# Performance work log

Hardware: AMD Instinct MI355X
Metric: run time of the kernel (lower is better)

The kernel has to match this reference:

```python
import jax, jax.numpy as jnp
import numpy as np
import math

D_MODEL = 768
D_STATE = 16
D_CONV = 4
EXPAND = 2
D_INNER = EXPAND * D_MODEL
DT_RANK = math.ceil(D_MODEL / 16)
B_SZ, SEQ = 2, 2048


def setup_inputs() -> dict:
    key = jax.random.key(0)
    ks = jax.random.split(key, 10)
    s = 0.02
    inp = {
        "input_states": jax.random.normal(ks[0], (B_SZ, SEQ, D_MODEL), jnp.float32),
        "in_proj_w": jax.random.normal(ks[1], (2 * D_INNER, D_MODEL), jnp.float32) * s,
        "conv_w": jax.random.normal(ks[2], (D_INNER, 1, D_CONV), jnp.float32) * s,
        "conv_b": jnp.zeros((D_INNER,), jnp.float32),
        "x_proj_w": jax.random.normal(ks[3], (DT_RANK + 2 * D_STATE, D_INNER), jnp.float32) * s,
        "dt_proj_w": jax.random.normal(ks[4], (D_INNER, DT_RANK), jnp.float32) * s,
        "dt_proj_b": jax.random.normal(ks[5], (D_INNER,), jnp.float32) * 0.1,
        # S4D-real style init: A_log = log(1..d_state) per channel
        "A_log": jnp.log(jnp.broadcast_to(jnp.arange(1, D_STATE + 1, dtype=jnp.float32), (D_INNER, D_STATE))),
        "D": jnp.ones((D_INNER,), jnp.float32),
        "out_proj_w": jax.random.normal(ks[6], (D_MODEL, D_INNER), jnp.float32) * s,
        "context_len": 2,
    }
    return inp


def _silu(x):
    return x * jax.nn.sigmoid(x)


def _chain_tree_scan(w, x):
    # first-order linear recurrence h_t = w_t * h_{t-1} + x_t along last axis
    # (w_0 is ignored by construction of the associative combine)
    def comb(l, r):
        al, bl = l
        ar, br = r
        return (ar * al, ar * bl + br)
    _, h = jax.lax.associative_scan(comb, (w, x), axis=-1)
    return h


def reference(input_states, in_proj_w, conv_w, conv_b, x_proj_w,
              dt_proj_w, dt_proj_b, A_log, D, out_proj_w, context_len):
    # context_len == 2 -> chain-tree branch (identity BFS order, parent[i]=i-1)
    b, L, dm = input_states.shape
    di, n = A_log.shape[0], A_log.shape[1]

    proj = jnp.einsum('bld,ed->ble', input_states, in_proj_w)  # [b,l,2*di]
    proj = jnp.transpose(proj, (0, 2, 1))                      # [b,2*di,l]
    hidden, gate = jnp.split(proj, 2, axis=1)                  # each [b,di,l]

    # causal depthwise conv1d (pad left d_conv-1, truncate to seq_len)
    hidden = jax.lax.conv_general_dilated(
        hidden, conv_w, window_strides=(1,), padding=[(D_CONV - 1, 0)],
        dimension_numbers=('NCH', 'OIH', 'NCH'), feature_group_count=di)
    hidden = _silu(hidden + conv_b[None, :, None])             # [b,di,l]

    ssm = jnp.einsum('bdl,ed->ble', hidden, x_proj_w)          # [b,l,dt_rank+2n]
    dt, Bm, Cm = jnp.split(ssm, [DT_RANK, DT_RANK + n], axis=-1)
    dt = jax.nn.softplus(jnp.einsum('blr,dr->bld', dt, dt_proj_w) + dt_proj_b)
    dt = jnp.transpose(dt, (0, 2, 1))                          # [b,di,l]

    A = -jnp.exp(A_log.astype(jnp.float32))                    # [di,n]
    dA = jnp.exp(A[None, :, None, :] * dt[:, :, :, None])      # [b,di,l,n]
    dBu = dt[:, :, :, None] * Bm[:, None, :, :] * hidden[:, :, :, None]  # [b,di,l,n]

    # rearrange 'b d l n -> b (d n) l'
    w = jnp.transpose(dA, (0, 1, 3, 2)).reshape(b, di * n, L)
    fin = jnp.transpose(dBu, (0, 1, 3, 2)).reshape(b, di * n, L)

    fin_f = jnp.flip(fin, axis=-1)
    w_f = jnp.roll(jnp.flip(w, axis=-1), 1, axis=-1)

    h = _chain_tree_scan(w_f, fin_f)
    # feature_out2 (edge_weight == w_f via identity gather) * 0.3 + feature_out1
    fout = 1.3 * h

    fout = jnp.flip(fout, axis=-1)                              # [b,(d n),l]
    fout = fout.reshape(b, di, n, L)
    fout = jnp.transpose(fout, (0, 3, 1, 2))                    # [b,l,d,n]

    scan_out = jnp.einsum('bldn,bln->bld', fout, Cm)            # [b,l,di]
    scan_out = jnp.transpose(scan_out, (0, 2, 1))               # [b,di,l]

    y = scan_out + hidden * D[None, :, None]
    y = y * _silu(gate)
    out = jnp.einsum('bdl,ed->ble', y, out_proj_w)              # [b,l,d_model]
    return out
```

## Files before the change

kernel.cpp:

```cpp
#include <hip/hip_runtime.h>
#include <hip/hip_bf16.h>

#define DI     1536
#define DM     768
#define E2     3072
#define NST    16
#define LSEQ   2048
#define NB     2
#define NLB    4096
#define SSMW   80
#define DTRANK 48
#define NC     32
#define CP     64
#define LOG2E  1.44269504f
#define RLOG2E 0.69314718f

typedef unsigned short u16;
typedef unsigned int   u32;
typedef __attribute__((ext_vector_type(8))) __bf16 bf16x8;
typedef __attribute__((ext_vector_type(4))) float  f32x4;

__device__ __forceinline__ float b2f(u16 u) {
  union { u32 i; float f; } v; v.i = ((u32)u) << 16; return v.f;
}
__device__ __forceinline__ u16 f2b(float f) {
  union { float f; u32 i; } v; v.f = f;
  u32 r = v.i + 0x7FFFu + ((v.i >> 16) & 1u);
  return (u16)(r >> 16);
}
__device__ __forceinline__ void gld16(const u16* g, u16* l) {
  __builtin_amdgcn_global_load_lds(
      (const __attribute__((address_space(1))) void*)g,
      (__attribute__((address_space(3))) void*)l, 16, 0, 0);
}
__device__ __forceinline__ float silu_f(float x) {
  return x / (1.f + __expf(-x));
}
__device__ __forceinline__ float fexp2(float x) { return __builtin_amdgcn_exp2f(x); }
__device__ __forceinline__ float flog2(float x) { return __builtin_amdgcn_logf(x); }
__device__ __forceinline__ float softplus_f(float x) {
  return (x > 20.f) ? x : flog2(1.f + fexp2(x * LOG2E)) * RLOG2E;
}

#define ROWSUM16(p)                                                                \
  asm("v_add_f32 %0, %0, %0 row_ror:8 row_mask:0xf bank_mask:0xf" : "+v"(p));      \
  asm("v_add_f32 %0, %0, %0 row_ror:4 row_mask:0xf bank_mask:0xf" : "+v"(p));      \
  asm("v_add_f32 %0, %0, %0 row_ror:2 row_mask:0xf bank_mask:0xf" : "+v"(p));      \
  asm("v_add_f32 %0, %0, %0 row_ror:1 row_mask:0xf bank_mask:0xf" : "+v"(p));

__global__ __launch_bounds__(256) void castall(const float* __restrict__ x_in,
                                               const float* __restrict__ w_in,
                                               const float* __restrict__ w_out,
                                               const float* __restrict__ w_x,
                                               const float* __restrict__ w_dt,
                                               const float* __restrict__ b_dt,
                                               u16* __restrict__ in_b,
                                               u16* __restrict__ win_b,
                                               u16* __restrict__ wout_b,
                                               u16* __restrict__ wx_b,
                                               u16* __restrict__ wdtp_b) {
  int i = (blockIdx.x * 256 + threadIdx.x) * 4;
  const int n1 = NLB * DM, n2 = n1 + E2 * DM, n3 = n2 + DM * DI, n4 = n3 + SSMW * DI;
  const int n5 = n4 + DI * 64;
  if (i >= n5) return;
  if (i >= n4) {
    int off = i - n4;
    u16 o[4];
#pragma unroll
    for (int j = 0; j < 4; j++) {
      int row = (off + j) >> 6, col = (off + j) & 63;
      float v = (col < 48) ? w_dt[row * 48 + col] : (col == 48 ? b_dt[row] : 0.f);
      o[j] = f2b(v);
    }
    uint2 pk; pk.x = (u32)o[0] | ((u32)o[1] << 16); pk.y = (u32)o[2] | ((u32)o[3] << 16);
    *(uint2*)(wdtp_b + off) = pk;
    return;
  }
  const float* src; u16* dst; int off;
  if (i < n1)      { src = x_in;  dst = in_b;   off = i; }
  else if (i < n2) { src = w_in;  dst = win_b;  off = i - n1; }
  else if (i < n3) { src = w_out; dst = wout_b; off = i - n2; }
  else             { src = w_x;   dst = wx_b;   off = i - n3; }
  float4 v = *(const float4*)(src + off);
  u32 lo = (u32)f2b(v.x) | ((u32)f2b(v.y) << 16);
  u32 hi = (u32)f2b(v.z) | ((u32)f2b(v.w) << 16);
  uint2 pk; pk.x = lo; pk.y = hi;
  *(uint2*)(dst + off) = pk;
}

template<int CMODE>
__global__ __launch_bounds__(256) void gemm_bt(const u16* __restrict__ A,
                                               const u16* __restrict__ B,
                                               void* __restrict__ Cp,
                                               int M, int N, int K) {
  __shared__ __align__(16) u16 a_s[128 * 32];
  __shared__ __align__(16) u16 b_s[128 * 32];
  const int tid = threadIdx.x, lane = tid & 63, w = tid >> 6;
  const int m0 = blockIdx.x * 128, n0 = blockIdx.y * 128;
  const int wm = w >> 1, wn = w & 1;
  f32x4 acc[4][4];
#pragma unroll
  for (int i = 0; i < 4; i++)
#pragma unroll
    for (int j = 0; j < 4; j++) acc[i][j] = (f32x4){0.f, 0.f, 0.f, 0.f};

  const int rA = lane >> 2;
  const int c8 = (lane & 3) * 8;
  const int fr = lane & 15;
  const int fk = (lane >> 4) * 8;

  for (int k0 = 0; k0 < K; k0 += 32) {
#pragma unroll
    for (int j = 0; j < 2; j++) {
      int rr = (w * 2 + j) * 16;
      gld16(A + (size_t)(m0 + rr + rA) * K + k0 + c8, a_s + rr * 32);
      gld16(B + (size_t)(n0 + rr + rA) * K + k0 + c8, b_s + rr * 32);
    }
    __syncthreads();
    bf16x8 af[4], bf[4];
#pragma unroll
    for (int mi = 0; mi < 4; mi++)
      af[mi] = *(const bf16x8*)(a_s + (wm * 64 + mi * 16 + fr) * 32 + fk);
#pragma unroll
    for (int ni = 0; ni < 4; ni++)
      bf[ni] = *(const bf16x8*)(b_s + (wn * 64 + ni * 16 + fr) * 32 + fk);
#pragma unroll
    for (int mi = 0; mi < 4; mi++)
#pragma unroll
      for (int ni = 0; ni < 4; ni++)
        acc[mi][ni] = __builtin_amdgcn_mfma_f32_16x16x32_bf16(
            af[mi], bf[ni], acc[mi][ni], 0, 0, 0);
    __syncthreads();
  }

  const int rbase = (lane >> 4) * 4, cbase = lane & 15;
#pragma unroll
  for (int mi = 0; mi < 4; mi++)
#pragma unroll
    for (int ni = 0; ni < 4; ni++)
#pragma unroll
      for (int j = 0; j < 4; j++) {
        int m = m0 + wm * 64 + mi * 16 + rbase + j;
        int n = n0 + wn * 64 + ni * 16 + cbase;
        float v = acc[mi][ni][j];
        if (CMODE == 0) {
          u16* C = (u16*)Cp;
          C[((size_t)(n >> 11) * E2 + m) * LSEQ + (n & 2047)] = f2b(v);
        } else {
          float* C = (float*)Cp;
          C[(size_t)m * N + n] = v;
        }
      }
}

__global__ __launch_bounds__(256) void gemm_xproj(const u16* __restrict__ A,
                                                  const u16* __restrict__ B,
                                                  float* __restrict__ C,
                                                  u16* __restrict__ dtin) {
  __shared__ __align__(16) u16 a_s[128 * 32];
  __shared__ __align__(16) u16 b_s[128 * 32];
  const int tid = threadIdx.x, lane = tid & 63, w = tid >> 6;
  const int n0 = blockIdx.x * 128;
  const int K = DI;
  f32x4 acc[5][2];
#pragma unroll
  for (int i = 0; i < 5; i++) { acc[i][0] = (f32x4){0,0,0,0}; acc[i][1] = (f32x4){0,0,0,0}; }

  const int rA = lane >> 2;
  const int c8 = (lane & 3) * 8;
  const int fr = lane & 15;
  const int fk = (lane >> 4) * 8;

  for (int k0 = 0; k0 < K; k0 += 32) {
#pragma unroll
    for (int j = 0; j < 2; j++) {
      int rr = (w * 2 + j) * 16;
      gld16(A + (size_t)(rr + rA) * K + k0 + c8, a_s + rr * 32);
      gld16(B + (size_t)(n0 + rr + rA) * K + k0 + c8, b_s + rr * 32);
    }
    __syncthreads();
    bf16x8 af[5], bf[2];
#pragma unroll
    for (int mi = 0; mi < 5; mi++)
      af[mi] = *(const bf16x8*)(a_s + (mi * 16 + fr) * 32 + fk);
#pragma unroll
    for (int ni = 0; ni < 2; ni++)
      bf[ni] = *(const bf16x8*)(b_s + (w * 32 + ni * 16 + fr) * 32 + fk);
#pragma unroll
    for (int mi = 0; mi < 5; mi++)
#pragma unroll
      for (int ni = 0; ni < 2; ni++)
        acc[mi][ni] = __builtin_amdgcn_mfma_f32_16x16x32_bf16(
            af[mi], bf[ni], acc[mi][ni], 0, 0, 0);
    __syncthreads();
  }

  const int rbase = (lane >> 4) * 4, cbase = lane & 15;
#pragma unroll
  for (int mi = 0; mi < 5; mi++)
#pragma unroll
    for (int ni = 0; ni < 2; ni++)
#pragma unroll
      for (int j = 0; j < 4; j++) {
        int m = mi * 16 + rbase + j;
        int n = n0 + w * 32 + ni * 16 + cbase;
        float v = acc[mi][ni][j];
        C[(size_t)n * SSMW + m] = v;
        if (m < 64) {
          u16 dv = (m < 48) ? f2b(v) : (m == 48 ? f2b(1.0f) : (u16)0);
          dtin[(size_t)n * 64 + m] = dv;
        }
      }
}

__global__ __launch_bounds__(256) void conv_silu(const u16* __restrict__ proj,
                                                 const float* __restrict__ cw,
                                                 const float* __restrict__ cb,
                                                 u16* __restrict__ hidden) {
  __shared__ __align__(16) u16 in_s[64][96];
  __shared__ __align__(16) u16 o_s[64][64];
  const int t = threadIdx.x;
  const int d0 = blockIdx.x * 64, l0 = blockIdx.y * 64, bb = blockIdx.z;

  for (int c = t; c < 64 * 12; c += 256) {
    int r = c / 12, q = c % 12;
    int gl = l0 - 32 + q * 8;
    uint4 v;
    if (gl >= 0) v = *(const uint4*)(proj + ((size_t)bb * E2 + d0 + r) * LSEQ + gl);
    else         v = (uint4){0u, 0u, 0u, 0u};
    *(uint4*)(&in_s[r][q * 8]) = v;
  }
  __syncthreads();

  const int dd = t >> 2, ls = t & 3;
  const int d = d0 + dd;
  const float w0 = cw[d * 4 + 0], w1 = cw[d * 4 + 1], w2 = cw[d * 4 + 2], w3 = cw[d * 4 + 3];
  const float bias = cb[d];
#pragma unroll
  for (int i = 0; i < 16; i++) {
    int li = ls * 16 + i;
    int base = 32 + li - 3;
    float h = w0 * b2f(in_s[dd][base + 0]) + w1 * b2f(in_s[dd][base + 1]) +
              w2 * b2f(in_s[dd][base + 2]) + w3 * b2f(in_s[dd][base + 3]) + bias;
    o_s[li][dd] = f2b(silu_f(h));
  }
  __syncthreads();

  for (int c = t; c < 512; c += 256) {
    int r = c >> 3, q = c & 7;
    *(uint4*)(hidden + ((size_t)bb * LSEQ + l0 + r) * DI + d0 + q * 8) =
        *(const uint4*)(&o_s[r][q * 8]);
  }
}


#define DT_TILE_MFMA(dtin, wdtp)                                                          \
  {                                                                                       \
    const u16* ar = dtin + ((size_t)bb * LSEQ + l0) * 64;                                 \
    bf16x8 wb0 = *(const bf16x8*)(wdtp + (size_t)(d0 + fr) * 64 + fk);                    \
    bf16x8 wb1 = *(const bf16x8*)(wdtp + (size_t)(d0 + fr) * 64 + 32 + fk);               \
    for (int mt = wv; mt < 5; mt += 4) {                                                  \
      bf16x8 a0 = *(const bf16x8*)(ar + (size_t)(mt * 16 + fr) * 64 + fk);                \
      bf16x8 a1 = *(const bf16x8*)(ar + (size_t)(mt * 16 + fr) * 64 + 32 + fk);           \
      f32x4 da = (f32x4){0.f, 0.f, 0.f, 0.f};                                             \
      da = __builtin_amdgcn_mfma_f32_16x16x32_bf16(a0, wb0, da, 0, 0, 0);                 \
      da = __builtin_amdgcn_mfma_f32_16x16x32_bf16(a1, wb1, da, 0, 0, 0);                 \
      _Pragma("unroll")                                                                   \
      for (int j = 0; j < 4; j++)                                                         \
        dt_f[cbase][mt * 16 + rbase + j] = softplus_f(da[j]);                             \
    }                                                                                     \
  }

__global__ __launch_bounds__(256) void scan_sum(const u16* __restrict__ dtin,
                                                const u16* __restrict__ wdtp,
                                                const u16* __restrict__ hidden,
                                                const float* __restrict__ ssm,
                                                const float* __restrict__ A_log,
                                                float* __restrict__ gsum,
                                                float* __restrict__ sdt) {
  __shared__ __align__(16) float dt_f[16][84];
  __shared__ __align__(16) float hid_f[16][68];
  __shared__ __align__(16) float B_t[16][68];
  const int t = threadIdx.x;
  const int d0 = blockIdx.x * 16, c = blockIdx.y, bb = blockIdx.z;
  const int dl = t >> 4, n = t & 15;
  const int d = d0 + dl;
  const int l0 = c * CP;
  const int lane = t & 63, wv = t >> 6;
  const int fr = lane & 15, fk = (lane >> 4) * 8;
  const int rbase = (lane >> 4) * 4, cbase = lane & 15;
  {
    int r = t >> 2, q = t & 3;
    size_t lbrow = (size_t)bb * LSEQ + l0 + r;
    uint2 hv = *(const uint2*)(hidden + lbrow * DI + d0 + q * 4);
    float4 bv = *(const float4*)(ssm + lbrow * SSMW + 48 + q * 4);
    hid_f[q * 4 + 0][r] = b2f((u16)hv.x); hid_f[q * 4 + 1][r] = b2f((u16)(hv.x >> 16));
    hid_f[q * 4 + 2][r] = b2f((u16)hv.y); hid_f[q * 4 + 3][r] = b2f((u16)(hv.y >> 16));
    B_t[q * 4 + 0][r] = bv.x; B_t[q * 4 + 1][r] = bv.y;
    B_t[q * 4 + 2][r] = bv.z; B_t[q * 4 + 3][r] = bv.w;
  }
  DT_TILE_MFMA(dtin, wdtp)
  const float An2 = -__expf(A_log[d * 16 + n]) * LOG2E;
  __syncthreads();
  float dt_prev = (c == NC - 1) ? 0.f : dt_f[dl][64];
  float g = 0.f, sumdt = 0.f;
#define STEPS(dtv_, hv_, Bv_) {            \
    float dtv = dtv_;                      \
    float dA = fexp2(An2 * dt_prev);       \
    g = dtv * (Bv_) * (hv_) + dA * g;      \
    sumdt += dt_prev;                      \
    dt_prev = dtv; }
#pragma unroll
  for (int s = 7; s >= 0; --s) {
    f32x4 t0 = *(const f32x4*)(&dt_f[dl][s * 8]);
    f32x4 t1 = *(const f32x4*)(&dt_f[dl][s * 8 + 4]);
    f32x4 h0 = *(const f32x4*)(&hid_f[dl][s * 8]);
    f32x4 h1 = *(const f32x4*)(&hid_f[dl][s * 8 + 4]);
    f32x4 b0 = *(const f32x4*)(&B_t[n][s * 8]);
    f32x4 b1 = *(const f32x4*)(&B_t[n][s * 8 + 4]);
    STEPS(t1[3], h1[3], b1[3]);
    STEPS(t1[2], h1[2], b1[2]);
    STEPS(t1[1], h1[1], b1[1]);
    STEPS(t1[0], h1[0], b1[0]);
    STEPS(t0[3], h0[3], b0[3]);
    STEPS(t0[2], h0[2], b0[2]);
    STEPS(t0[1], h0[1], b0[1]);
    STEPS(t0[0], h0[0], b0[0]);
  }
#undef STEPS
  size_t idx = (((size_t)bb * NC + c) * DI + d) * 16 + n;
  gsum[idx] = g;
  sdt[idx]  = sumdt;
}

__global__ __launch_bounds__(256) void scan_carry(const float* __restrict__ gsum,
                                                  const float* __restrict__ sdt,
                                                  const float* __restrict__ A_log,
                                                  float* __restrict__ carry) {
  const int t = blockIdx.x * 256 + threadIdx.x;
  const int bb = blockIdx.y;
  const int d = t >> 4, n = t & 15;
  const float An2 = -__expf(A_log[d * 16 + n]) * LOG2E;
  float cg = 0.f;
  carry[(((size_t)bb * NC + NC - 1) * DI + d) * 16 + n] = 0.f;
  for (int c = NC - 2; c >= 0; --c) {
    size_t up = (((size_t)bb * NC + (c + 1)) * DI + d) * 16 + n;
    cg = gsum[up] + fexp2(An2 * sdt[up]) * cg;
    carry[(((size_t)bb * NC + c) * DI + d) * 16 + n] = cg;
  }
}

__global__ __launch_bounds__(256) void scan_apply(const u16* __restrict__ proj,
                                                  const u16* __restrict__ hidden,
                                                  const u16* __restrict__ dtin,
                                                  const u16* __restrict__ wdtp,
                                                  const float* __restrict__ ssm,
                                                  const float* __restrict__ A_log,
                                                  const float* __restrict__ Dp,
                                                  const float* __restrict__ carry,
                                                  u16* __restrict__ y) {
  __shared__ __align__(16) float dt_f[16][84];
  __shared__ __align__(16) float hid_f[16][68];
  __shared__ __align__(16) float B_t[16][68];
  __shared__ __align__(16) float C_t[16][68];
  __shared__ __align__(16) u16 gate_t[16][80];
  __shared__ __align__(16) u16 y_s[64][16];
  const int t = threadIdx.x;
  const int d0 = blockIdx.x * 16, c = blockIdx.y, bb = blockIdx.z;
  const int dl = t >> 4, n = t & 15;
  const int d = d0 + dl;
  const int l0 = c * CP;
  const int lane = t & 63, wv = t >> 6;
  const int fr = lane & 15, fk = (lane >> 4) * 8;
  const int rbase = (lane >> 4) * 4, cbase = lane & 15;
  {
    int r = t >> 2, q = t & 3;
    size_t lbrow = (size_t)bb * LSEQ + l0 + r;
    uint2 hv = *(const uint2*)(hidden + lbrow * DI + d0 + q * 4);
    float4 bv = *(const float4*)(ssm + lbrow * SSMW + 48 + q * 4);
    float4 cv = *(const float4*)(ssm + lbrow * SSMW + 64 + q * 4);
    hid_f[q * 4 + 0][r] = b2f((u16)hv.x); hid_f[q * 4 + 1][r] = b2f((u16)(hv.x >> 16));
    hid_f[q * 4 + 2][r] = b2f((u16)hv.y); hid_f[q * 4 + 3][r] = b2f((u16)(hv.y >> 16));
    B_t[q * 4 + 0][r] = bv.x; B_t[q * 4 + 1][r] = bv.y;
    B_t[q * 4 + 2][r] = bv.z; B_t[q * 4 + 3][r] = bv.w;
    C_t[q * 4 + 0][r] = cv.x; C_t[q * 4 + 1][r] = cv.y;
    C_t[q * 4 + 2][r] = cv.z; C_t[q * 4 + 3][r] = cv.w;
  }
  {
    int r = t >> 4, q = t & 15;
    *(uint2*)(&gate_t[r][q * 4]) =
        *(const uint2*)(proj + ((size_t)bb * E2 + DI + d0 + r) * LSEQ + l0 + q * 4);
  }
  DT_TILE_MFMA(dtin, wdtp)
  const float An2 = -__expf(A_log[d * 16 + n]) * LOG2E;
  const float Dd = Dp[d];
  float g = carry[(((size_t)bb * NC + c) * DI + d) * 16 + n];
  __syncthreads();
  float dt_prev = (c == NC - 1) ? 0.f : dt_f[dl][64];
  float pcap[4] = {0.f, 0.f, 0.f, 0.f};
#define STEPA(IDX, dtv_, hv_, Bv_, Cv_) {                  \
    float dtv = dtv_;                                      \
    float dA = fexp2(An2 * dt_prev);                       \
    g = dtv * (Bv_) * (hv_) + dA * g;                      \
    float p = g * (Cv_);                                   \
    ROWSUM16(p);                                           \
    if (n == ((IDX) & 15)) pcap[(IDX) >> 4] = p;           \
    dt_prev = dtv; }
#pragma unroll
  for (int s = 7; s >= 0; --s) {
    f32x4 t0 = *(const f32x4*)(&dt_f[dl][s * 8]);
    f32x4 t1 = *(const f32x4*)(&dt_f[dl][s * 8 + 4]);
    f32x4 h0 = *(const f32x4*)(&hid_f[dl][s * 8]);
    f32x4 h1 = *(const f32x4*)(&hid_f[dl][s * 8 + 4]);
    f32x4 b0 = *(const f32x4*)(&B_t[n][s * 8]);
    f32x4 b1 = *(const f32x4*)(&B_t[n][s * 8 + 4]);
    f32x4 c0 = *(const f32x4*)(&C_t[n][s * 8]);
    f32x4 c1 = *(const f32x4*)(&C_t[n][s * 8 + 4]);
    STEPA(s * 8 + 7, t1[3], h1[3], b1[3], c1[3]);
    STEPA(s * 8 + 6, t1[2], h1[2], b1[2], c1[2]);
    STEPA(s * 8 + 5, t1[1], h1[1], b1[1], c1[1]);
    STEPA(s * 8 + 4, t1[0], h1[0], b1[0], c1[0]);
    STEPA(s * 8 + 3, t0[3], h0[3], b0[3], c0[3]);
    STEPA(s * 8 + 2, t0[2], h0[2], b0[2], c0[2]);
    STEPA(s * 8 + 1, t0[1], h0[1], b0[1], c0[1]);
    STEPA(s * 8 + 0, t0[0], h0[0], b0[0], c0[0]);
  }
#undef STEPA
#pragma unroll
  for (int j2 = 0; j2 < 4; ++j2) {
    float hval = hid_f[dl][n + 16 * j2];
    float gv = b2f(gate_t[dl][n + 16 * j2]);
    float yv = (1.3f * pcap[j2] + hval * Dd) * silu_f(gv);
    y_s[n + 16 * j2][dl] = f2b(yv);
  }
  __syncthreads();
  {
    int r = t >> 2, q = t & 3;
    *(uint2*)(y + ((size_t)bb * LSEQ + l0 + r) * DI + d0 + q * 4) =
        *(const uint2*)(&y_s[r][q * 4]);
  }
}

extern "C" void kernel_launch(void* const* d_in, const int* in_sizes, int n_in,
                              void* d_out, int out_size, void* d_ws, size_t ws_size,
                              hipStream_t stream) {
  const float* x_in   = (const float*)d_in[0];
  const float* w_in   = (const float*)d_in[1];
  const float* conv_w = (const float*)d_in[2];
  const float* conv_b = (const float*)d_in[3];
  const float* w_x    = (const float*)d_in[4];
  const float* w_dt   = (const float*)d_in[5];
  const float* b_dt   = (const float*)d_in[6];
  const float* A_log  = (const float*)d_in[7];
  const float* Dp     = (const float*)d_in[8];
  const float* w_out  = (const float*)d_in[9];
  float* outp = (float*)d_out;

  size_t off = 0;
  auto carve = [&](size_t bytes) {
    void* p = (char*)d_ws + off;
    off += (bytes + 255) & ~(size_t)255;
    return p;
  };
  u16*   in_b   = (u16*)  carve((size_t)NLB * DM * 2);
  u16*   win_b  = (u16*)  carve((size_t)E2 * DM * 2);
  u16*   wout_b = (u16*)  carve((size_t)DM * DI * 2);
  u16*   wx_b   = (u16*)  carve((size_t)SSMW * DI * 2);
  u16*   wdtp_b = (u16*)  carve((size_t)DI * 64 * 2);
  u16*   proj_b = (u16*)  carve((size_t)NB * E2 * LSEQ * 2);
  u16*   hid_b  = (u16*)  carve((size_t)NLB * DI * 2);
  float* ssm_b  = (float*)carve((size_t)NLB * SSMW * 4);
  u16*   dtin_b = (u16*)  carve((size_t)(NLB + 64) * 64 * 2);
  u16*   y_b    = (u16*)  carve((size_t)NLB * DI * 2);
  float* gsum_b = (float*)carve((size_t)NB * NC * DI * 16 * 4);
  float* sdt_b  = (float*)carve((size_t)NB * NC * DI * 16 * 4);
  float* car_b  = (float*)carve((size_t)NB * NC * DI * 16 * 4);

  const int ncast = NLB * DM + E2 * DM + DM * DI + SSMW * DI + DI * 64;
  castall<<<(ncast + 1023) / 1024, 256, 0, stream>>>(
      x_in, w_in, w_out, w_x, w_dt, b_dt, in_b, win_b, wout_b, wx_b, wdtp_b);

  gemm_bt<0><<<dim3(E2 / 128, NLB / 128), 256, 0, stream>>>(
      win_b, in_b, proj_b, E2, NLB, DM);
  conv_silu<<<dim3(DI / 64, LSEQ / 64, NB), 256, 0, stream>>>(
      proj_b, conv_w, conv_b, hid_b);
  gemm_xproj<<<NLB / 128, 256, 0, stream>>>(wx_b, hid_b, ssm_b, dtin_b);

  scan_sum<<<dim3(DI / 16, NC, NB), 256, 0, stream>>>(
      dtin_b, wdtp_b, hid_b, ssm_b, A_log, gsum_b, sdt_b);
  scan_carry<<<dim3(DI * 16 / 256, NB), 256, 0, stream>>>(
      gsum_b, sdt_b, A_log, car_b);
  scan_apply<<<dim3(DI / 16, NC, NB), 256, 0, stream>>>(
      proj_b, hid_b, dtin_b, wdtp_b, ssm_b, A_log, Dp, car_b, y_b);

  gemm_bt<1><<<dim3(NLB / 128, DM / 128), 256, 0, stream>>>(
      y_b, wout_b, outp, NLB, DM, DI);
}
```

Measured before the change: 285.9 us.

## Remap GEMM workgroup ids across XCDs and use scalar capture registers in scan

The GEMM kernel now permutes the linear block id so that consecutive tiles land on the same XCD (round-robin over 8 chiplets), aiming at better L2 reuse of shared A/B tiles. The scan kernel replaces the pcap array, indexed by (IDX>>4), with four named scalars filled by explicitly unrolled macros. This keeps the captured values in registers and avoids scratch spills or dynamic indexing. The remap assumes the grid size is divisible by 8; otherwise some tiles would be skipped or duplicated.

```diff
diff --git a/kernel.cpp b/kernel.cpp
--- a/kernel.cpp
+++ b/kernel.cpp
@@ -96,7 +96,10 @@
   __shared__ __align__(16) u16 a_s[128 * 32];
   __shared__ __align__(16) u16 b_s[128 * 32];
   const int tid = threadIdx.x, lane = tid & 63, w = tid >> 6;
-  const int m0 = blockIdx.x * 128, n0 = blockIdx.y * 128;
+  const int orig = blockIdx.y * gridDim.x + blockIdx.x;
+  const int cpx = (gridDim.x * gridDim.y) >> 3;
+  const int wgid = (orig & 7) * cpx + (orig >> 3);
+  const int m0 = (wgid % gridDim.x) * 128, n0 = (wgid / gridDim.x) * 128;
   const int wm = w >> 1, wn = w & 1;
   f32x4 acc[4][4];
 #pragma unroll
@@ -397,42 +400,48 @@
   float g = carry[(((size_t)bb * NC + c) * DI + d) * 16 + n];
   __syncthreads();
   float dt_prev = (c == NC - 1) ? 0.f : dt_f[dl][64];
-  float pcap[4] = {0.f, 0.f, 0.f, 0.f};
-#define STEPA(IDX, dtv_, hv_, Bv_, Cv_) {                  \
+
+#define STEP1(IDX, dtv_, hv_, Bv_, Cv_, PC) {              \
     float dtv = dtv_;                                      \
     float dA = fexp2(An2 * dt_prev);                       \
     g = dtv * (Bv_) * (hv_) + dA * g;                      \
     float p = g * (Cv_);                                   \
     ROWSUM16(p);                                           \
-    if (n == ((IDX) & 15)) pcap[(IDX) >> 4] = p;           \
+    if (n == ((IDX) & 15)) PC = p;                         \
     dt_prev = dtv; }
-#pragma unroll
-  for (int s = 7; s >= 0; --s) {
-    f32x4 t0 = *(const f32x4*)(&dt_f[dl][s * 8]);
-    f32x4 t1 = *(const f32x4*)(&dt_f[dl][s * 8 + 4]);
-    f32x4 h0 = *(const f32x4*)(&hid_f[dl][s * 8]);
-    f32x4 h1 = *(const f32x4*)(&hid_f[dl][s * 8 + 4]);
-    f32x4 b0 = *(const f32x4*)(&B_t[n][s * 8]);
-    f32x4 b1 = *(const f32x4*)(&B_t[n][s * 8 + 4]);
-    f32x4 c0 = *(const f32x4*)(&C_t[n][s * 8]);
-    f32x4 c1 = *(const f32x4*)(&C_t[n][s * 8 + 4]);
-    STEPA(s * 8 + 7, t1[3], h1[3], b1[3], c1[3]);
-    STEPA(s * 8 + 6, t1[2], h1[2], b1[2], c1[2]);
-    STEPA(s * 8 + 5, t1[1], h1[1], b1[1], c1[1]);
-    STEPA(s * 8 + 4, t1[0], h1[0], b1[0], c1[0]);
-    STEPA(s * 8 + 3, t0[3], h0[3], b0[3], c0[3]);
-    STEPA(s * 8 + 2, t0[2], h0[2], b0[2], c0[2]);
-    STEPA(s * 8 + 1, t0[1], h0[1], b0[1], c0[1]);
-    STEPA(s * 8 + 0, t0[0], h0[0], b0[0], c0[0]);
-  }
-#undef STEPA
-#pragma unroll
-  for (int j2 = 0; j2 < 4; ++j2) {
-    float hval = hid_f[dl][n + 16 * j2];
-    float gv = b2f(gate_t[dl][n + 16 * j2]);
-    float yv = (1.3f * pcap[j2] + hval * Dd) * silu_f(gv);
-    y_s[n + 16 * j2][dl] = f2b(yv);
-  }
+#define STEP8(S, PC) {                                          \
+    f32x4 t0 = *(const f32x4*)(&dt_f[dl][(S) * 8]);             \
+    f32x4 t1 = *(const f32x4*)(&dt_f[dl][(S) * 8 + 4]);         \
+    f32x4 h0 = *(const f32x4*)(&hid_f[dl][(S) * 8]);            \
+    f32x4 h1 = *(const f32x4*)(&hid_f[dl][(S) * 8 + 4]);        \
+    f32x4 b0 = *(const f32x4*)(&B_t[n][(S) * 8]);               \
+    f32x4 b1 = *(const f32x4*)(&B_t[n][(S) * 8 + 4]);           \
+    f32x4 c0 = *(const f32x4*)(&C_t[n][(S) * 8]);               \
+    f32x4 c1 = *(const f32x4*)(&C_t[n][(S) * 8 + 4]);           \
+    STEP1((S) * 8 + 7, t1[3], h1[3], b1[3], c1[3], PC);         \
+    STEP1((S) * 8 + 6, t1[2], h1[2], b1[2], c1[2], PC);         \
+    STEP1((S) * 8 + 5, t1[1], h1[1], b1[1], c1[1], PC);         \
+    STEP1((S) * 8 + 4, t1[0], h1[0], b1[0], c1[0], PC);         \
+    STEP1((S) * 8 + 3, t0[3], h0[3], b0[3], c0[3], PC);         \
+    STEP1((S) * 8 + 2, t0[2], h0[2], b0[2], c0[2], PC);         \
+    STEP1((S) * 8 + 1, t0[1], h0[1], b0[1], c0[1], PC);         \
+    STEP1((S) * 8 + 0, t0[0], h0[0], b0[0], c0[0], PC);         \
+  }
+  float p3 = 0.f, p2 = 0.f, p1 = 0.f, p0 = 0.f;
+  STEP8(7, p3) STEP8(6, p3)
+  STEP8(5, p2) STEP8(4, p2)
+  STEP8(3, p1) STEP8(2, p1)
+  STEP8(1, p0) STEP8(0, p0)
+#undef STEP8
+#undef STEP1
+
+#define EPI(J, P) {                                        \
+    float hval = hid_f[dl][n + 16 * (J)];                  \
+    float gv = b2f(gate_t[dl][n + 16 * (J)]);              \
+    float yv = (1.3f * (P) + hval * Dd) * silu_f(gv);      \
+    y_s[n + 16 * (J)][dl] = f2b(yv); }
+  EPI(0, p0) EPI(1, p1) EPI(2, p2) EPI(3, p3)
+#undef EPI
   __syncthreads();
   {
     int r = t >> 2, q = t & 3;
```

After: 284.7 us. Within noise of the previous version (-0.4%).
